# Performance work log

Hardware: AMD Instinct MI355X
Metric: run time of the kernel (lower is better)

The kernel has to match this reference:

```python
import jax, jax.numpy as jnp
import numpy as np

B, N, D, H = 2, 2048, 768, 12
HD = D // H


def setup_inputs() -> dict:
    key = jax.random.key(0)
    ks = jax.random.split(key, 8)
    x = jax.random.normal(ks[0], (B, N, D), dtype=jnp.float32)
    dist = jax.random.randint(ks[1], (B, N, N), 0, 32, dtype=jnp.int32)
    mask = jax.random.bernoulli(ks[2], 0.1, (B, N))  # True = masked key
    # parameters (torch Linear stored pre-transposed: y = x @ W + b)
    s = 1.0 / np.sqrt(D)
    qkv_w = jax.random.uniform(ks[3], (D, 3 * D), jnp.float32, -s, s)
    qkv_b = jax.random.uniform(ks[4], (3 * D,), jnp.float32, -s, s)
    out_w = jax.random.uniform(ks[5], (D, D), jnp.float32, -s, s)
    out_b = jax.random.uniform(ks[6], (D,), jnp.float32, -s, s)
    bias_table = jax.random.normal(ks[7], (32, H), dtype=jnp.float32)
    return {"x": x, "dist": dist, "mask": mask, "qkv_w": qkv_w,
            "qkv_b": qkv_b, "out_w": out_w, "out_b": out_b,
            "bias_table": bias_table}


def reference(x, dist, mask, qkv_w, qkv_b, out_w, out_b, bias_table):
    scale = HD ** -0.5
    qkv = x @ qkv_w + qkv_b                      # [B,N,3D]
    q, k, v = jnp.split(qkv, 3, axis=-1)
    sh = lambda t: t.reshape(B, N, H, HD).transpose(0, 2, 1, 3)  # [B,H,N,HD]
    q, k, v = sh(q), sh(k), sh(v)
    a = jnp.einsum('bhnd,bhmd->bhnm', q, k) * scale  # [B,H,N,N]
    # relative-position bias: gather [B,N,N,H] -> [B,H,N,N]
    a = a + bias_table[jnp.clip(dist, 0, 31)].transpose(0, 3, 1, 2)
    a = jnp.where(mask[:, None, None, :], -jnp.inf, a)
    a = jax.nn.softmax(a.astype(jnp.float32), axis=-1)  # dropout: eval mode (p ignored)
    o = jnp.einsum('bhnm,bhmd->bhnd', a, v)            # [B,H,N,HD]
    o = o.transpose(0, 2, 1, 3).reshape(B, N, D)
    return o @ out_w + out_b
```

## Files before the change

### kernel.cpp

```cpp
#include <hip/hip_runtime.h>
#include <hip/hip_bf16.h>

typedef unsigned short u16;
typedef __attribute__((ext_vector_type(8))) short bf16x8;
typedef __attribute__((ext_vector_type(4))) short bf16x4;
typedef __attribute__((ext_vector_type(4))) float f32x4;

#define MFMA_BF16(a,b,c) __builtin_amdgcn_mfma_f32_16x16x32_bf16((a),(b),(c),0,0,0)
#define LOG2E 1.4426950408889634f

#if __has_builtin(__builtin_amdgcn_mfma_f32_16x16x16bf16_1k)
#define MFMA16(a,b,c) __builtin_amdgcn_mfma_f32_16x16x16bf16_1k((a),(b),(c),0,0,0)
#define HAVE_MFMA16 1
#elif __has_builtin(__builtin_amdgcn_mfma_f32_16x16x16_bf16)
#define MFMA16(a,b,c) __builtin_amdgcn_mfma_f32_16x16x16_bf16((a),(b),(c),0,0,0)
#define HAVE_MFMA16 1
#else
#define HAVE_MFMA16 0
#endif

__device__ __forceinline__ u16 f2b(float f) {
    __hip_bfloat16 h = __float2bfloat16(f);
    u16 u; __builtin_memcpy(&u, &h, 2); return u;
}
__device__ __forceinline__ f32x4 zero4() { f32x4 z = {0.f,0.f,0.f,0.f}; return z; }

__device__ __forceinline__ void gl_lds16(const u16* g, u16* l) {
    __builtin_amdgcn_global_load_lds(
        (const __attribute__((address_space(1))) unsigned int*)g,
        (__attribute__((address_space(3))) unsigned int*)l,
        16, 0, 0);
}

__global__ __launch_bounds__(256) void convX(const float* __restrict__ in, u16* __restrict__ out) {
    size_t i = ((size_t)blockIdx.x * 256 + threadIdx.x) * 8;
    float4 a = *(const float4*)(in + i);
    float4 b = *(const float4*)(in + i + 4);
    union { u16 s[8]; uint4 v; } u;
    u.s[0]=f2b(a.x); u.s[1]=f2b(a.y); u.s[2]=f2b(a.z); u.s[3]=f2b(a.w);
    u.s[4]=f2b(b.x); u.s[5]=f2b(b.y); u.s[6]=f2b(b.z); u.s[7]=f2b(b.w);
    *(uint4*)(out + i) = u.v;
}

__global__ __launch_bounds__(256) void packDist(const int* __restrict__ din,
                                                const unsigned long long* __restrict__ mbits,
                                                unsigned char* __restrict__ dout) {
    size_t i = ((size_t)blockIdx.x * 256 + threadIdx.x) * 4;
    int4 v = *(const int4*)(din + i);
    int b = (int)(i >> 22);
    int j = (int)(i & 2047);
    unsigned bits = (unsigned)((mbits[b*32 + (j >> 6)] >> (j & 63)) & 0xFull);
    uchar4 o;
    o.x = (bits & 1u) ? 32 : (unsigned char)min(max(v.x, 0), 31);
    o.y = (bits & 2u) ? 32 : (unsigned char)min(max(v.y, 0), 31);
    o.z = (bits & 4u) ? 32 : (unsigned char)min(max(v.z, 0), 31);
    o.w = (bits & 8u) ? 32 : (unsigned char)min(max(v.w, 0), 31);
    *(uchar4*)(dout + i) = o;
}

__global__ __launch_bounds__(256) void convTW(const float* __restrict__ in, u16* __restrict__ out, int C) {
    __shared__ __align__(16) u16 T[64][68];
    int c0 = blockIdx.x * 64, k0 = blockIdx.y * 64;
    int tid = threadIdx.x;
#pragma unroll
    for (int i = 0; i < 4; ++i) {
        int id = tid + i * 256;
        int row = id >> 4, ch = id & 15;
        float4 v = *(const float4*)(in + (size_t)(k0 + row) * C + c0 + ch * 4);
        T[row][ch*4+0] = f2b(v.x); T[row][ch*4+1] = f2b(v.y);
        T[row][ch*4+2] = f2b(v.z); T[row][ch*4+3] = f2b(v.w);
    }
    __syncthreads();
#pragma unroll
    for (int i = 0; i < 2; ++i) {
        int id = tid + i * 256;
        int c = id >> 3, ch = id & 7;
        union { u16 s[8]; uint4 v; } u;
#pragma unroll
        for (int j = 0; j < 8; ++j) u.s[j] = T[ch*8+j][c];
        *(uint4*)(out + (size_t)(c0 + c) * 768 + k0 + ch * 8) = u.v;
    }
}

__global__ void detectMaskBits(const unsigned* __restrict__ m, unsigned long long* __restrict__ mbits) {
    __shared__ int sB, sH, sF;
    if (threadIdx.x == 0) { sB = 0; sH = 0; sF = 0; }
    __syncthreads();
    int lb = 0, lh = 0, lf = 0;
#pragma unroll
    for (int i = 0; i < 4; ++i) {
        unsigned v = m[threadIdx.x + i * 256];
        if (v == 0x3f800000u) { lf = 1; }
        else if (v > 1u) {
            unsigned b0 = v & 0xffu, b1 = (v >> 8) & 0xffu, b2 = (v >> 16) & 0xffu, b3 = v >> 24;
            bool bytesOK = (b0 <= 1u) && (b1 <= 1u) && (b2 <= 1u) && (b3 <= 1u);
            unsigned h0 = v & 0xffffu, h1 = v >> 16;
            bool halfOK = (h0 == 0u || h0 == 0x3f80u) && (h1 == 0u || h1 == 0x3f80u);
            if (bytesOK) lb = 1; else if (halfOK) lh = 1;
        }
    }
    if (lb) atomicOr(&sB, 1);
    if (lh) atomicOr(&sH, 1);
    if (lf) atomicOr(&sF, 1);
    __syncthreads();
    int mode = sH ? 3 : (sB ? 1 : (sF ? 2 : 0));
    const unsigned char* m8 = (const unsigned char*)m;
    const u16* mh = (const u16*)m;
    const float* mf = (const float*)m;
    const int* mi = (const int*)m;
    for (int it = 0; it < 16; ++it) {
        int e = it * 256 + threadIdx.x;
        int pred;
        if (mode == 0)      pred = (mi[e] != 0);
        else if (mode == 1) pred = (m8[e] != 0);
        else if (mode == 2) pred = (mf[e] != 0.0f);
        else                pred = (mh[e] != 0);
        unsigned long long bal = __ballot(pred);
        if ((threadIdx.x & 63) == 0) mbits[it * 4 + (threadIdx.x >> 6)] = bal;
    }
}

template<int MODE>
__global__ __launch_bounds__(256)
void gemmBT(const u16* __restrict__ A, const u16* __restrict__ Bt,
            const float* __restrict__ bias,
            u16* __restrict__ qO, u16* __restrict__ kO, u16* __restrict__ vO,
            float* __restrict__ fO) {
    __shared__ __align__(16) u16 As[128][40];
    __shared__ __align__(16) u16 Bs[128][40];
    const int K = 768;
    const int tid = threadIdx.x;
    const int lane = tid & 63, w = tid >> 6;
    const int wm = w >> 1, wn = w & 1;
    const int l15 = lane & 15, q = lane >> 4;
    const int m0 = blockIdx.y * 128, n0 = blockIdx.x * 128;
    const int rowS = tid >> 1, cS = (tid & 1) * 2;
    const u16* Ag = A + (size_t)(m0 + rowS) * K;
    const u16* Bg = Bt + (size_t)(n0 + rowS) * K;
    uint4 pa0, pa1, pb0, pb1;
    { const uint4* sa = (const uint4*)Ag; pa0 = sa[cS]; pa1 = sa[cS+1];
      const uint4* sb = (const uint4*)Bg; pb0 = sb[cS]; pb1 = sb[cS+1]; }
    f32x4 acc[4][4];
#pragma unroll
    for (int i=0;i<4;++i)
#pragma unroll
        for (int j=0;j<4;++j) acc[i][j] = zero4();

    for (int kt = 0; kt < 24; ++kt) {
        __syncthreads();
        *(uint4*)&As[rowS][cS*8]   = pa0; *(uint4*)&As[rowS][cS*8+8] = pa1;
        *(uint4*)&Bs[rowS][cS*8]   = pb0; *(uint4*)&Bs[rowS][cS*8+8] = pb1;
        __syncthreads();
        if (kt < 23) {
            const uint4* sa = (const uint4*)(Ag + (kt+1)*32);
            pa0 = sa[cS]; pa1 = sa[cS+1];
            const uint4* sb = (const uint4*)(Bg + (kt+1)*32);
            pb0 = sb[cS]; pb1 = sb[cS+1];
        }
        bf16x8 af[4], bfr[4];
#pragma unroll
        for (int mt=0; mt<4; ++mt) af[mt]  = *(const bf16x8*)&As[wm*64+mt*16+l15][q*8];
#pragma unroll
        for (int nt=0; nt<4; ++nt) bfr[nt] = *(const bf16x8*)&Bs[wn*64+nt*16+l15][q*8];
#pragma unroll
        for (int mt=0; mt<4; ++mt)
#pragma unroll
            for (int nt=0; nt<4; ++nt)
                acc[mt][nt] = MFMA_BF16(af[mt], bfr[nt], acc[mt][nt]);
    }

#pragma unroll
    for (int mt=0; mt<4; ++mt) {
#pragma unroll
        for (int nt=0; nt<4; ++nt) {
            int n = n0 + wn*64 + nt*16 + l15;
            float bv = bias[n];
            if (MODE == 0) {
                int which = n / 768;
                int rem = n - which*768;
                int hh = rem >> 6, hd = rem & 63;
                int mBase = m0 + wm*64 + mt*16 + q*4;
                int b = mBase >> 11, tok0 = mBase & 2047;
                if (which == 2) {
                    union { u16 s4[4]; unsigned long long u; } pv;
#pragma unroll
                    for (int r=0; r<4; ++r) pv.s4[r] = f2b(acc[mt][nt][r] + bv);
                    *(unsigned long long*)(vO + ((size_t)(b*12 + hh)*64 + hd)*2048 + tok0) = pv.u;
                } else {
#pragma unroll
                    for (int r=0; r<4; ++r) {
                        float v = acc[mt][nt][r] + bv;
                        size_t di = (((size_t)(b*12 + hh))*2048 + tok0 + r)*64 + hd;
                        if (which == 0) qO[di] = f2b(v * (0.125f * LOG2E));
                        else            kO[di] = f2b(v);
                    }
                }
            } else {
#pragma unroll
                for (int r=0; r<4; ++r) {
                    int m = m0 + wm*64 + mt*16 + q*4 + r;
                    fO[(size_t)m*768 + n] = acc[mt][nt][r] + bv;
                }
            }
        }
    }
}

__global__ __launch_bounds__(256)
void flashAttn(const u16* __restrict__ Qb, const u16* __restrict__ Kb,
               const u16* __restrict__ Vt, const unsigned char* __restrict__ dist8,
               const float* __restrict__ btg, u16* __restrict__ attnout) {
    __shared__ float bt[33];
    __shared__ __align__(16) u16 KT[2][4096];
    __shared__ __align__(16) u16 VT[2][4096];
    __shared__ __align__(16) u16 Os[4][16][72];
    const int tid = threadIdx.x;
    const int lane = tid & 63, w = tid >> 6;
    const int l15 = lane & 15, q = lane >> 4;
    const int wg = blockIdx.x + 32 * (blockIdx.y + 12 * blockIdx.z);
    const int xcd = wg & 7, slot = wg >> 3;
    const int g = ((slot >> 5) << 3) + xcd;
    const int i0 = (slot & 31) * 64;
    const int b = g / 12, h = g - b * 12;
    const int bh = g;
    const float NEG_INF = -__builtin_inff();
    if (tid < 33) bt[tid] = (tid == 32) ? NEG_INF : btg[tid*12 + h] * LOG2E;

    const int iRow = i0 + w*16 + l15;
    const u16* Qp = Qb + ((size_t)bh*2048 + iRow)*64;
    bf16x8 qB0 = *(const bf16x8*)(Qp + q*8);
    bf16x8 qB1 = *(const bf16x8*)(Qp + 32 + q*8);
    const unsigned char* dp = dist8 + ((size_t)(b*2048 + iRow))*2048 + q*4;
#if !HAVE_MFMA16
    const int srcL0 = ((2*q)   & 3)*16 + l15;
    const int srcL1 = ((2*q+1) & 3)*16 + l15;
    union { unsigned u4[4]; bf16x8 v; } one_;
    { unsigned oc = (l15 == 0) ? 0x3F803F80u : 0u;
      one_.u4[0]=oc; one_.u4[1]=oc; one_.u4[2]=oc; one_.u4[3]=oc; }
#else
    union { unsigned u2[2]; bf16x4 v; } one4_;
    { unsigned oc = (l15 == 0) ? 0x3F803F80u : 0u;
      one4_.u2[0]=oc; one4_.u2[1]=oc; }
#endif

    const int stRow = w*16 + (lane >> 3);
    const int stCol = (((lane & 7) ^ (lane >> 3)) << 4);
    const char* kgB = (const char*)Kb + (size_t)bh*2048*128;
    const char* vgB = (const char*)Vt + (size_t)bh*64*4096;
    const int swz = (l15 & 7) << 4;
    const int f0 = (q*16)      ^ swz;
    const int f1 = (q*16 + 64) ^ swz;
    const int rB = l15 * 128;

    {
        u16* kd = &KT[0][0] + w*1024;
        u16* vd = &VT[0][0] + w*1024;
#pragma unroll
        for (int c = 0; c < 2; ++c) {
            int row = stRow + c*8;
            gl_lds16((const u16*)(kgB + (size_t)row*128 + stCol),  kd + c*512);
            gl_lds16((const u16*)(vgB + (size_t)row*4096 + stCol), vd + c*512);
        }
    }
    __syncthreads();

    f32x4 o0 = zero4(), o1 = zero4(), o2 = zero4(), o3 = zero4(), o4 = zero4();
    float mI = NEG_INF;
    int cur = 0;

    for (int jt = 0; jt < 32; ++jt) {
        const int j0 = jt * 64;
        if (jt < 31) {
            const int j0n = j0 + 64;
            u16* kd = &KT[cur^1][0] + w*1024;
            u16* vd = &VT[cur^1][0] + w*1024;
#pragma unroll
            for (int c = 0; c < 2; ++c) {
                int row = stRow + c*8;
                gl_lds16((const u16*)(kgB + (size_t)(j0n + row)*128 + stCol),          kd + c*512);
                gl_lds16((const u16*)(vgB + (size_t)row*4096 + (size_t)j0n*2 + stCol), vd + c*512);
            }
        }
        unsigned dv4[4];
#pragma unroll
        for (int mt = 0; mt < 4; ++mt) dv4[mt] = *(const unsigned*)(dp + j0 + mt*16);

        const char* kt = (const char*)&KT[cur][0];
        f32x4 s0 = zero4(), s1 = zero4(), s2 = zero4(), s3 = zero4();
        {
            bf16x8 k00 = *(const bf16x8*)(kt + rB          + f0);
            bf16x8 k01 = *(const bf16x8*)(kt + rB          + f1);
            bf16x8 k10 = *(const bf16x8*)(kt + rB + 2048   + f0);
            bf16x8 k11 = *(const bf16x8*)(kt + rB + 2048   + f1);
            bf16x8 k20 = *(const bf16x8*)(kt + rB + 4096   + f0);
            bf16x8 k21 = *(const bf16x8*)(kt + rB + 4096   + f1);
            bf16x8 k30 = *(const bf16x8*)(kt + rB + 6144   + f0);
            bf16x8 k31 = *(const bf16x8*)(kt + rB + 6144   + f1);
            __builtin_amdgcn_s_setprio(1);
            s0 = MFMA_BF16(k00, qB0, s0); s0 = MFMA_BF16(k01, qB1, s0);
            s1 = MFMA_BF16(k10, qB0, s1); s1 = MFMA_BF16(k11, qB1, s1);
            s2 = MFMA_BF16(k20, qB0, s2); s2 = MFMA_BF16(k21, qB1, s2);
            s3 = MFMA_BF16(k30, qB0, s3); s3 = MFMA_BF16(k31, qB1, s3);
            __builtin_amdgcn_s_setprio(0);
        }

        float sv[4][4];
#pragma unroll
        for (int mt = 0; mt < 4; ++mt) {
            const f32x4 sm = mt==0 ? s0 : (mt==1 ? s1 : (mt==2 ? s2 : s3));
            const unsigned d4 = dv4[mt];
#pragma unroll
            for (int r = 0; r < 4; ++r) {
                int dd = (d4 >> (r*8)) & 255;
                sv[mt][r] = sm[r] + bt[dd];
            }
        }

        float t0 = fmaxf(fmaxf(sv[0][0], sv[0][1]), fmaxf(sv[0][2], sv[0][3]));
        float t1 = fmaxf(fmaxf(sv[1][0], sv[1][1]), fmaxf(sv[1][2], sv[1][3]));
        float t2 = fmaxf(fmaxf(sv[2][0], sv[2][1]), fmaxf(sv[2][2], sv[2][3]));
        float t3 = fmaxf(fmaxf(sv[3][0], sv[3][1]), fmaxf(sv[3][2], sv[3][3]));
        float rm = fmaxf(fmaxf(t0, t1), fmaxf(t2, t3));
        rm = fmaxf(rm, __shfl_xor(rm, 16, 64));
        rm = fmaxf(rm, __shfl_xor(rm, 32, 64));
        if (!__all(rm <= mI)) {
            float mn = fmaxf(mI, rm);
            float al = exp2f(mI - mn);
            mI = mn;
#pragma unroll
            for (int r = 0; r < 4; ++r) { o0[r] *= al; o1[r] *= al; o2[r] *= al; o3[r] *= al; }
            o4[0] *= al;
        }
        float p[4][4];
#pragma unroll
        for (int mt = 0; mt < 4; ++mt)
#pragma unroll
            for (int r = 0; r < 4; ++r) p[mt][r] = exp2f(sv[mt][r] - mI);

        const char* vt = (const char*)&VT[cur][0];
#if HAVE_MFMA16
        __builtin_amdgcn_s_setprio(1);
#pragma unroll
        for (int mt = 0; mt < 4; ++mt) {
            union { unsigned d[2]; bf16x4 v; } pu;
            pu.d[0] = (unsigned)f2b(p[mt][0]) | ((unsigned)f2b(p[mt][1]) << 16);
            pu.d[1] = (unsigned)f2b(p[mt][2]) | ((unsigned)f2b(p[mt][3]) << 16);
            const int cbase = (((mt*2 + (q>>1)) ^ (l15 & 7)) << 4) + (q & 1)*8;
            bf16x4 v0 = *(const bf16x4*)(vt + rB          + cbase);
            bf16x4 v1 = *(const bf16x4*)(vt + rB + 2048   + cbase);
            bf16x4 v2 = *(const bf16x4*)(vt + rB + 4096   + cbase);
            bf16x4 v3 = *(const bf16x4*)(vt + rB + 6144   + cbase);
            o0 = MFMA16(v0, pu.v, o0);
            o1 = MFMA16(v1, pu.v, o1);
            o2 = MFMA16(v2, pu.v, o2);
            o3 = MFMA16(v3, pu.v, o3);
            o4 = MFMA16(one4_.v, pu.v, o4);
        }
        __builtin_amdgcn_s_setprio(0);
#else
        unsigned pk[4][2];
#pragma unroll
        for (int mt = 0; mt < 4; ++mt) {
            pk[mt][0] = (unsigned)f2b(p[mt][0]) | ((unsigned)f2b(p[mt][1]) << 16);
            pk[mt][1] = (unsigned)f2b(p[mt][2]) | ((unsigned)f2b(p[mt][3]) << 16);
        }
        __builtin_amdgcn_s_setprio(1);
#pragma unroll
        for (int ks = 0; ks < 2; ++ks) {
            union { unsigned d[4]; bf16x8 v; } pb;
#pragma unroll
            for (int s = 0; s < 4; ++s) {
                int sl = (s >> 1) ? srcL1 : srcL0;
                int u0 = __shfl((int)pk[2*ks    ][s & 1], sl, 64);
                int u1 = __shfl((int)pk[2*ks + 1][s & 1], sl, 64);
                pb.d[s] = (q >> 1) ? (unsigned)u1 : (unsigned)u0;
            }
            const int fk = ks ? f1 : f0;
            bf16x8 v0 = *(const bf16x8*)(vt + rB          + fk);
            bf16x8 v1 = *(const bf16x8*)(vt + rB + 2048   + fk);
            bf16x8 v2 = *(const bf16x8*)(vt + rB + 4096   + fk);
            bf16x8 v3 = *(const bf16x8*)(vt + rB + 6144   + fk);
            o0 = MFMA_BF16(v0, pb.v, o0);
            o1 = MFMA_BF16(v1, pb.v, o1);
            o2 = MFMA_BF16(v2, pb.v, o2);
            o3 = MFMA_BF16(v3, pb.v, o3);
            o4 = MFMA_BF16(one_.v, pb.v, o4);
        }
        __builtin_amdgcn_s_setprio(0);
#endif

        __syncthreads();
        cur ^= 1;
    }

    float lsum = __shfl(o4[0], l15, 64);
    float inv = 1.0f / lsum;
#pragma unroll
    for (int r = 0; r < 4; ++r) {
        Os[w][l15][ 0 + q*4 + r] = f2b(o0[r] * inv);
        Os[w][l15][16 + q*4 + r] = f2b(o1[r] * inv);
        Os[w][l15][32 + q*4 + r] = f2b(o2[r] * inv);
        Os[w][l15][48 + q*4 + r] = f2b(o3[r] * inv);
    }
    __syncthreads();
    int rr = lane >> 2, cc = lane & 3;
    uint4 a0 = *(const uint4*)&Os[w][rr][cc*16];
    uint4 a1 = *(const uint4*)&Os[w][rr][cc*16 + 8];
    size_t orow = ((size_t)b*2048 + i0 + w*16 + rr)*768 + h*64 + cc*16;
    *(uint4*)(attnout + orow)     = a0;
    *(uint4*)(attnout + orow + 8) = a1;
}

extern "C" void kernel_launch(void* const* d_in, const int* in_sizes, int n_in,
                              void* d_out, int out_size, void* d_ws, size_t ws_size,
                              hipStream_t stream) {
    (void)in_sizes; (void)n_in; (void)out_size; (void)ws_size;
    const float* x      = (const float*)d_in[0];
    const int*   dist   = (const int*)d_in[1];
    const int*   mask   = (const int*)d_in[2];
    const float* qkv_w  = (const float*)d_in[3];
    const float* qkv_b  = (const float*)d_in[4];
    const float* out_w  = (const float*)d_in[5];
    const float* out_b  = (const float*)d_in[6];
    const float* btab   = (const float*)d_in[7];
    float* out = (float*)d_out;

    char* ws = (char*)d_ws;
    size_t off = 0;
    auto alloc = [&](size_t bytes) { void* p = ws + off; off += (bytes + 255) & ~(size_t)255; return p; };
    u16* xb      = (u16*)alloc((size_t)4096*768*2);
    u16* wqkvT   = (u16*)alloc((size_t)2304*768*2);
    u16* woutT   = (u16*)alloc((size_t)768*768*2);
    u16* Qb      = (u16*)alloc((size_t)24*2048*64*2);
    u16* Kb      = (u16*)alloc((size_t)24*2048*64*2);
    u16* Vtp     = (u16*)alloc((size_t)24*2048*64*2);
    u16* attnout = (u16*)alloc((size_t)4096*768*2);
    unsigned char* dist8 = (unsigned char*)alloc((size_t)2*2048*2048);
    unsigned long long* mbits = (unsigned long long*)alloc(64*8);

    convX<<<1536, 256, 0, stream>>>(x, xb);
    detectMaskBits<<<1, 256, 0, stream>>>((const unsigned*)mask, mbits);
    packDist<<<8192, 256, 0, stream>>>(dist, mbits, dist8);
    convTW<<<dim3(36,12), 256, 0, stream>>>(qkv_w, wqkvT, 2304);
    convTW<<<dim3(12,12), 256, 0, stream>>>(out_w, woutT, 768);
    gemmBT<0><<<dim3(18,32), 256, 0, stream>>>(xb, wqkvT, qkv_b, Qb, Kb, Vtp, nullptr);
    flashAttn<<<dim3(32,12,2), 256, 0, stream>>>(Qb, Kb, Vtp, dist8, btab, attnout);
    gemmBT<1><<<dim3(6,32), 256, 0, stream>>>(attnout, woutT, out_b, nullptr, nullptr, nullptr, out);
}
```

Measured before the change: 252.1 us.

## Double-buffer GEMM tiles with direct global-to-LDS loads and XOR swizzle

Replaces the register-staged single-buffer LDS tiles in the projection GEMM with double-buffered LDS filled by direct global-to-LDS loads (gl_lds16). An XOR swizzle on the 16-byte chunk index replaces the padded row stride to avoid bank conflicts. The goal is to overlap the next k-tile's load with the current MFMA work and to drop one barrier per iteration. It relies on the gl_lds16 helper defined elsewhere and on correct wait/barrier semantics for async LDS writes.

```diff
diff --git a/kernel.cpp b/kernel.cpp
--- a/kernel.cpp
+++ b/kernel.cpp
@@ -126,47 +126,61 @@
             const float* __restrict__ bias,
             u16* __restrict__ qO, u16* __restrict__ kO, u16* __restrict__ vO,
             float* __restrict__ fO) {
-    __shared__ __align__(16) u16 As[128][40];
-    __shared__ __align__(16) u16 Bs[128][40];
+    __shared__ __align__(16) u16 As[2][128*32];
+    __shared__ __align__(16) u16 Bs[2][128*32];
     const int K = 768;
     const int tid = threadIdx.x;
     const int lane = tid & 63, w = tid >> 6;
     const int wm = w >> 1, wn = w & 1;
     const int l15 = lane & 15, q = lane >> 4;
     const int m0 = blockIdx.y * 128, n0 = blockIdx.x * 128;
-    const int rowS = tid >> 1, cS = (tid & 1) * 2;
-    const u16* Ag = A + (size_t)(m0 + rowS) * K;
-    const u16* Bg = Bt + (size_t)(n0 + rowS) * K;
-    uint4 pa0, pa1, pb0, pb1;
-    { const uint4* sa = (const uint4*)Ag; pa0 = sa[cS]; pa1 = sa[cS+1];
-      const uint4* sb = (const uint4*)Bg; pb0 = sb[cS]; pb1 = sb[cS+1]; }
+    const int stRow = (lane >> 2);
+    const int stChunk = (lane & 3) ^ ((lane >> 3) & 3);
+    const u16* Ag = A + (size_t)(m0 + w*32 + stRow) * K + stChunk * 8;
+    const u16* Bg = Bt + (size_t)(n0 + w*32 + stRow) * K + stChunk * 8;
+    u16* ldsA = &As[0][0] + w*32*32;
+    u16* ldsB = &Bs[0][0] + w*32*32;
+    const int fA = (q ^ ((l15 >> 1) & 3)) * 8;
+
     f32x4 acc[4][4];
 #pragma unroll
     for (int i=0;i<4;++i)
 #pragma unroll
         for (int j=0;j<4;++j) acc[i][j] = zero4();
 
+#pragma unroll
+    for (int c = 0; c < 2; ++c) {
+        gl_lds16(Ag + (size_t)(c*16) * K, ldsA + c*16*32);
+        gl_lds16(Bg + (size_t)(c*16) * K, ldsB + c*16*32);
+    }
+    __syncthreads();
+
+    int cur = 0;
     for (int kt = 0; kt < 24; ++kt) {
-        __syncthreads();
-        *(uint4*)&As[rowS][cS*8]   = pa0; *(uint4*)&As[rowS][cS*8+8] = pa1;
-        *(uint4*)&Bs[rowS][cS*8]   = pb0; *(uint4*)&Bs[rowS][cS*8+8] = pb1;
-        __syncthreads();
         if (kt < 23) {
-            const uint4* sa = (const uint4*)(Ag + (kt+1)*32);
-            pa0 = sa[cS]; pa1 = sa[cS+1];
-            const uint4* sb = (const uint4*)(Bg + (kt+1)*32);
-            pb0 = sb[cS]; pb1 = sb[cS+1];
-        }
+            const int ko = (kt + 1) * 32;
+            u16* dA = &As[cur^1][0] + w*32*32;
+            u16* dB = &Bs[cur^1][0] + w*32*32;
+#pragma unroll
+            for (int c = 0; c < 2; ++c) {
+                gl_lds16(Ag + (size_t)(c*16) * K + ko, dA + c*16*32);
+                gl_lds16(Bg + (size_t)(c*16) * K + ko, dB + c*16*32);
+            }
+        }
+        const u16* as = &As[cur][0];
+        const u16* bs = &Bs[cur][0];
         bf16x8 af[4], bfr[4];
 #pragma unroll
-        for (int mt=0; mt<4; ++mt) af[mt]  = *(const bf16x8*)&As[wm*64+mt*16+l15][q*8];
-#pragma unroll
-        for (int nt=0; nt<4; ++nt) bfr[nt] = *(const bf16x8*)&Bs[wn*64+nt*16+l15][q*8];
+        for (int mt=0; mt<4; ++mt) af[mt]  = *(const bf16x8*)(as + (wm*64+mt*16+l15)*32 + fA);
+#pragma unroll
+        for (int nt=0; nt<4; ++nt) bfr[nt] = *(const bf16x8*)(bs + (wn*64+nt*16+l15)*32 + fA);
 #pragma unroll
         for (int mt=0; mt<4; ++mt)
 #pragma unroll
             for (int nt=0; nt<4; ++nt)
                 acc[mt][nt] = MFMA_BF16(af[mt], bfr[nt], acc[mt][nt]);
+        __syncthreads();
+        cur ^= 1;
     }
 
 #pragma unroll
```

After: 254.2 us. About the same (+0.8%).
